# Optimization experiments

Measured on AMD Instinct MI355X. Metric: run time of the kernel, lower is better.

The kernel has to match this reference:

```python
import jax, jax.numpy as jnp
import numpy as np
import math


def setup_inputs() -> dict:
    key = jax.random.key(0)
    ks = jax.random.split(key, 4)
    B, C, H, W, D = 16, 512, 64, 64, 256
    return {
        "x": jax.random.normal(ks[0], (B, C, H, W), jnp.float32),
        "weight_global": jax.random.normal(ks[1], (C, D), jnp.float32) * 0.02,  # trunc_normal std=0.02
        "conv_g_w": jax.random.normal(ks[2], (C, C), jnp.float32) * 0.02,       # 1x1 conv, no bias
        "bn_g_gamma": jnp.ones((C,), jnp.float32),
        "bn_g_beta": jnp.zeros((C,), jnp.float32),
        "conv_c_w": jax.random.normal(ks[3], (C, C), jnp.float32) * 0.02,
        "bn_c_gamma": jnp.ones((C,), jnp.float32),
        "bn_c_beta": jnp.zeros((C,), jnp.float32),
    }


def _bn(x, gamma, beta, eps=1e-5):
    # BatchNorm2d in default training mode: batch statistics over (B, H, W)
    mean = x.mean(axis=(0, 2, 3), keepdims=True)
    var = x.var(axis=(0, 2, 3), keepdims=True)
    xn = (x - mean) * jax.lax.rsqrt(var + eps)
    return xn * gamma[None, :, None, None] + beta[None, :, None, None]


def reference(x, weight_global, conv_g_w, bn_g_gamma, bn_g_beta, conv_c_w, bn_c_gamma, bn_c_beta):
    b, c, h, w = x.shape
    inv_sqrt_c = 1.0 / math.sqrt(c)

    # Description: QR-orthogonal codebook, Q: (c, d)
    Q, _ = jnp.linalg.qr(weight_global + 1e-8)

    # global branch: 1x1 conv -> BN -> ReLU -> global avg pool
    gx = jnp.einsum('oc,bchw->bohw', conv_g_w, x)
    gx = jax.nn.relu(_bn(gx, bn_g_gamma, bn_g_beta))
    g = gx.mean(axis=(2, 3))                                  # (b, c)
    aff_g = jax.nn.softmax((g @ Q) * inv_sqrt_c, axis=1)      # (b, d)
    g = jax.nn.sigmoid(aff_g @ Q.T)                           # (b, c)

    # channel branch: 1x1 conv -> BN -> ReLU
    cx = jnp.einsum('oc,bchw->bohw', conv_c_w, x)
    cx = jax.nn.relu(_bn(cx, bn_c_gamma, bn_c_beta))
    ch = cx.reshape(b, c, h * w).transpose(0, 2, 1)           # (b, hw, c)
    aff_c = jax.nn.softmax((ch @ Q) * inv_sqrt_c, axis=2)     # (b, hw, d)
    # sum(diag_embed(aff_c) @ Q.T, dim=2) == aff_c @ Q.T (fused, avoids (b,hw,d,c) intermediate)
    ch = aff_c @ Q.T                                          # (b, hw, c)

    o = ch * g[:, None, :]
    o = o.transpose(0, 2, 1).reshape(b, c, h, w)
    return o + x
```

## Files before the change

kernel.cpp:

```cpp
#include <hip/hip_runtime.h>
#include <hip/hip_bf16.h>

#define BB 16
#define CC 512
#define HWP 4096
#define DD 256
#define NPIX 65536
#define INV_SQRT_C 0.04419417382415922f

typedef unsigned short u16;
typedef __attribute__((ext_vector_type(8))) short s16x8;
typedef __attribute__((ext_vector_type(8))) unsigned short u16x8;
typedef __attribute__((ext_vector_type(4))) unsigned short u16x4;
typedef __attribute__((ext_vector_type(4))) float f32x4;

__device__ __forceinline__ u16 f2b(float f){
  unsigned int u = __builtin_bit_cast(unsigned int, f);
  unsigned int r = (u + 0x7fffu + ((u >> 16) & 1u)) >> 16;
  return (u16)r;
}

__device__ __forceinline__ f32x4 mfma16(s16x8 a, s16x8 b, f32x4 c){
  return __builtin_amdgcn_mfma_f32_16x16x32_bf16(a, b, c, 0, 0, 0);
}

__global__ __launch_bounds__(256) void k_xbar(const float* __restrict__ x, float* __restrict__ xbar){
  int c = blockIdx.x, tid = threadIdx.x;
  float s = 0.f;
  for (int b = 0; b < BB; ++b){
    const float* px = x + ((size_t)(b*CC + c))*HWP;
    for (int p = tid; p < HWP; p += 256) s += px[p];
  }
  __shared__ float red[256];
  red[tid] = s; __syncthreads();
  for (int st = 128; st; st >>= 1){ if (tid < st) red[tid] += red[tid+st]; __syncthreads(); }
  if (tid == 0) xbar[c] = red[0] * (1.0f/ (float)NPIX);
}

__global__ __launch_bounds__(512) void k_gram(const float* __restrict__ x, float* __restrict__ Spart, int kspl){
  __shared__ __align__(16) u16 Asl[128*72];
  __shared__ __align__(16) u16 Bsl[128*72];
  int tid = threadIdx.x;
  int w = tid >> 6, lane = tid & 63, lr = lane & 15, g = lane >> 4;
  int b = blockIdx.y;
  int kz = blockIdx.z;
  int t = blockIdx.x, ti = 0, rem = 4;
  while (t >= rem){ t -= rem; ++ti; --rem; }
  int tj = ti + t;
  int r0 = ti*128, c0 = tj*128;
  int wm = w >> 2, wn = w & 3;
  f32x4 acc[4][2] = {};
  const float* xb = x + (size_t)b*CC*HWP;
  int klen = HWP / kspl;
  int kbase = kz * klen;
  for (int k0 = kbase; k0 < kbase + klen; k0 += 64){
    __syncthreads();
    for (int tt = tid; tt < 4096; tt += 512){
      int arr = tt >> 11;
      int row = (tt >> 4) & 127;
      int q = tt & 15;
      const float* src = xb + (size_t)((arr ? c0 : r0) + row)*HWP + k0 + q*4;
      f32x4 v = *(const f32x4*)src;
      u16x4 u; u[0]=f2b(v[0]); u[1]=f2b(v[1]); u[2]=f2b(v[2]); u[3]=f2b(v[3]);
      u16* dst = (arr ? Bsl : Asl) + row*72 + q*4;
      *(u16x4*)dst = u;
    }
    __syncthreads();
    #pragma unroll
    for (int kc = 0; kc < 2; ++kc){
      s16x8 av[4], bv[2];
      #pragma unroll
      for (int mt = 0; mt < 4; ++mt) av[mt] = *(const s16x8*)&Asl[(wm*64 + mt*16 + lr)*72 + kc*32 + g*8];
      #pragma unroll
      for (int nt = 0; nt < 2; ++nt) bv[nt] = *(const s16x8*)&Bsl[(wn*32 + nt*16 + lr)*72 + kc*32 + g*8];
      #pragma unroll
      for (int mt = 0; mt < 4; ++mt)
        #pragma unroll
        for (int nt = 0; nt < 2; ++nt)
          acc[mt][nt] = mfma16(av[mt], bv[nt], acc[mt][nt]);
    }
  }
  float* sp = Spart + (size_t)(b*kspl + kz)*262144;
  #pragma unroll
  for (int mt = 0; mt < 4; ++mt)
    #pragma unroll
    for (int nt = 0; nt < 2; ++nt)
      #pragma unroll
      for (int r = 0; r < 4; ++r)
        sp[(size_t)(r0 + wm*64 + mt*16 + 4*g + r)*512 + c0 + wn*32 + nt*16 + lr] = acc[mt][nt][r];
}

__global__ __launch_bounds__(256) void k_sreduce(const float* __restrict__ Spart, float* __restrict__ S, int nslots){
  int idx = blockIdx.x*256 + threadIdx.x;
  int i = idx >> 9, j = idx & 511;
  int src = ((i >> 7) <= (j >> 7)) ? idx : (j*512 + i);
  float s = 0.f;
  for (int k = 0; k < nslots; ++k) s += Spart[(size_t)k*262144 + src];
  S[idx] = s;
}

__global__ __launch_bounds__(256) void k_G(const float* __restrict__ wg, float* __restrict__ G){
  int i = blockIdx.x, j = threadIdx.x;
  float s = 0.f;
  for (int c = 0; c < CC; ++c)
    s = fmaf(wg[c*DD + i] + 1e-8f, wg[c*DD + j] + 1e-8f, s);
  G[i*DD + j] = s;
}

__global__ __launch_bounds__(256) void k_cholPanel(float* __restrict__ G, int kb){
  int tid = threadIdx.x;
  int lane = tid & 63;
  int j = lane & 31;
  int K0 = kb*32;
  float c[32];
  #pragma unroll
  for (int i = 0; i < 32; ++i)
    c[i] = (i <= j) ? G[(K0+i)*DD + K0 + j] : 0.f;
  #pragma unroll
  for (int k = 0; k < 32; ++k){
    float piv = __shfl(c[k], k);
    float sd = sqrtf(piv);
    float ukj = c[k] / sd;
    c[k] = ukj;
    float uk[32];
    #pragma unroll
    for (int i = k + 1; i < 32; ++i) uk[i] = __shfl(ukj, i);
    #pragma unroll
    for (int i = k + 1; i < 32; ++i) c[i] -= uk[i] * ukj;
  }
  if (tid < 32){
    #pragma unroll
    for (int i = 0; i < 32; ++i)
      if (i <= j) G[(K0+i)*DD + K0 + j] = c[i];
  }
  int nt = 256 - K0 - 32;
  int jg = K0 + 32 + tid;
  if (tid < nt){
    float y[32];
    #pragma unroll
    for (int i = 0; i < 32; ++i) y[i] = G[(K0+i)*DD + jg];
    #pragma unroll
    for (int i = 0; i < 32; ++i){
      float s0 = y[i];
      #pragma unroll
      for (int l = 0; l < 32; ++l)
        if (l < i) s0 -= __shfl(c[l], i) * y[l];
      y[i] = s0 / __shfl(c[i], i);
    }
    #pragma unroll
    for (int i = 0; i < 32; ++i) G[(K0+i)*DD + jg] = y[i];
  }
}

__global__ __launch_bounds__(256) void k_cholTrail(float* __restrict__ G, int kb){
  int K0 = kb*32;
  int nt = 256 - K0 - 32;
  int T = (nt + 63) >> 6;
  int t = blockIdx.x, ti = 0, rem = T;
  while (t >= rem){ t -= rem; ++ti; --rem; }
  int tj = ti + t;
  int r0 = K0 + 32 + ti*64;
  int c0 = K0 + 32 + tj*64;
  __shared__ __align__(16) float Ur[32][64];
  __shared__ __align__(16) float Uc[32][64];
  int tid = threadIdx.x;
  for (int idx = tid; idx < 2048; idx += 256){
    int k = idx >> 6, cc = idx & 63;
    int gr = r0 + cc, gc = c0 + cc;
    Ur[k][cc] = (gr < 256) ? G[(K0+k)*DD + gr] : 0.f;
    Uc[k][cc] = (gc < 256) ? G[(K0+k)*DD + gc] : 0.f;
  }
  __syncthreads();
  int tr = (tid >> 4) * 4;
  int tc = (tid & 15) * 4;
  float acc[4][4] = {};
  #pragma unroll
  for (int k = 0; k < 32; ++k){
    f32x4 a = *(const f32x4*)&Ur[k][tr];
    f32x4 b = *(const f32x4*)&Uc[k][tc];
    #pragma unroll
    for (int ii = 0; ii < 4; ++ii)
      #pragma unroll
      for (int jj = 0; jj < 4; ++jj)
        acc[ii][jj] += a[ii]*b[jj];
  }
  #pragma unroll
  for (int ii = 0; ii < 4; ++ii){
    int gi = r0 + tr + ii;
    if (gi >= 256) continue;
    #pragma unroll
    for (int jj = 0; jj < 4; ++jj){
      int gj = c0 + tc + jj;
      if (gj < 256 && gj >= gi)
        G[gi*DD + gj] -= acc[ii][jj];
    }
  }
}

__global__ __launch_bounds__(256) void k_qsolve(const float* __restrict__ G,
    const float* __restrict__ wg,
    float* __restrict__ Q, float* __restrict__ Qst,
    u16* __restrict__ Qb, u16* __restrict__ Qstb){
  __shared__ __align__(16) float Pp[8192];
  __shared__ float Qlds[256*64];
  __shared__ float Wred[3*32*64];
  int tid = threadIdx.x;
  int w = tid >> 6, lane = tid & 63;
  int c = blockIdx.x*64 + lane;
  const float* arow = wg + (size_t)c*DD;

  for (int J = 0; J < 8; ++J){
    int J0 = J*32;
    int nrows8 = (J0 + 32)*8;
    for (int idx = tid; idx < nrows8; idx += 256){
      int row = idx >> 3, q = idx & 7;
      *(f32x4*)&Pp[row*32 + q*4] = *(const f32x4*)&G[row*256 + J0 + q*4];
    }
    __syncthreads();

    float W[32];
    if (w == 0){
      #pragma unroll
      for (int r = 0; r < 32; ++r) W[r] = arow[J0 + r] + 1e-8f;
    } else {
      #pragma unroll
      for (int r = 0; r < 32; ++r) W[r] = 0.f;
    }
    for (int M = w; M < J; M += 4){
      #pragma unroll 4
      for (int k = 0; k < 32; ++k){
        int row = M*32 + k;
        float qv = Qlds[row*64 + lane];
        const float* pr = &Pp[row*32];
        #pragma unroll
        for (int r4 = 0; r4 < 8; ++r4){
          f32x4 p = *(const f32x4*)&pr[r4*4];
          W[r4*4+0] -= qv*p[0];
          W[r4*4+1] -= qv*p[1];
          W[r4*4+2] -= qv*p[2];
          W[r4*4+3] -= qv*p[3];
        }
      }
    }
    if (w > 0){
      #pragma unroll
      for (int r = 0; r < 32; ++r) Wred[((w-1)*32 + r)*64 + lane] = W[r];
    }
    __syncthreads();

    if (w == 0){
      #pragma unroll
      for (int r = 0; r < 32; ++r)
        W[r] += Wred[r*64 + lane] + Wred[(32+r)*64 + lane] + Wred[(64+r)*64 + lane];
      #pragma unroll
      for (int i = 0; i < 32; ++i){
        float t = W[i];
        for (int l = 0; l < i; ++l) t -= W[l] * Pp[(J0 + l)*32 + i];
        W[i] = t / Pp[(J0 + i)*32 + i];
      }
      #pragma unroll
      for (int i = 0; i < 32; ++i) Qlds[(J0 + i)*64 + lane] = W[i];
      #pragma unroll
      for (int r4 = 0; r4 < 8; ++r4){
        f32x4 q4; u16x4 qb4;
        #pragma unroll
        for (int jj = 0; jj < 4; ++jj){ q4[jj] = W[r4*4+jj]; qb4[jj] = f2b(W[r4*4+jj]); }
        *(f32x4*)&Q[(size_t)c*DD + J0 + r4*4] = q4;
        *(u16x4*)&Qb[(size_t)c*DD + J0 + r4*4] = qb4;
      }
      #pragma unroll
      for (int i = 0; i < 32; ++i){
        float qs = W[i] * INV_SQRT_C;
        Qst[(size_t)(J0 + i)*CC + c] = qs;
        Qstb[(size_t)(J0 + i)*CC + c] = f2b(qs);
      }
    }
    __syncthreads();
  }
}

__global__ __launch_bounds__(256) void k_fold(const float* __restrict__ Wg, const float* __restrict__ Wc,
    const float* __restrict__ gamg, const float* __restrict__ betg,
    const float* __restrict__ gamc, const float* __restrict__ betc,
    const float* __restrict__ S, const float* __restrict__ xbar,
    float* __restrict__ Wgf, float* __restrict__ bgf,
    float* __restrict__ Wcf, float* __restrict__ bcf,
    u16* __restrict__ Wgb, u16* __restrict__ Wcb){
  int o = blockIdx.x & 511, br = blockIdx.x >> 9;
  int tid = threadIdx.x;
  const float* W = br ? Wc : Wg;
  __shared__ float wrow[512];
  __shared__ float red[256];
  __shared__ float red2[256];
  __shared__ float sc_s, bi_s;
  wrow[tid] = W[o*512 + tid]; wrow[tid+256] = W[o*512 + tid + 256];
  __syncthreads();
  float mp = 0.f;
  for (int c = tid; c < 512; c += 256) mp = fmaf(wrow[c], xbar[c], mp);
  float qp = 0.f;
  for (int c1 = tid; c1 < 512; c1 += 256){
    const float* srow = S + (size_t)c1*512;
    float y = 0.f;
    for (int c2 = 0; c2 < 512; ++c2) y = fmaf(srow[c2], wrow[c2], y);
    qp = fmaf(wrow[c1], y, qp);
  }
  red[tid] = mp; red2[tid] = qp; __syncthreads();
  for (int st = 128; st; st >>= 1){
    if (tid < st){ red[tid] += red[tid+st]; red2[tid] += red2[tid+st]; }
    __syncthreads();
  }
  if (tid == 0){
    float m = red[0];
    float E = red2[0] * (1.0f/(float)NPIX);
    float var = E - m*m;
    float rstd = rsqrtf(var + 1e-5f);
    float gma = br ? gamc[o] : gamg[o];
    float bta = br ? betc[o] : betg[o];
    sc_s = gma * rstd;
    bi_s = bta - gma * rstd * m;
  }
  __syncthreads();
  float* Wf = br ? Wcf : Wgf;
  float* bf = br ? bcf : bgf;
  u16* Wb  = br ? Wcb : Wgb;
  float w0 = sc_s * wrow[tid], w1 = sc_s * wrow[tid+256];
  Wf[o*512 + tid]     = w0;
  Wf[o*512 + tid+256] = w1;
  Wb[o*512 + tid]     = f2b(w0);
  Wb[o*512 + tid+256] = f2b(w1);
  if (tid == 0) bf[o] = bi_s;
}

__global__ __launch_bounds__(512) void k_gconv(const float* __restrict__ x,
    const u16* __restrict__ Wb, const float* __restrict__ bf, float* __restrict__ gpart){
  __shared__ __align__(16) u16 Xs[64*512];
  int tid = threadIdx.x;
  int w = tid >> 6, lane = tid & 63, lr = lane & 15, g = lane >> 4;
  int slab = blockIdx.x, b = blockIdx.y;
  int p0 = slab*64;

  {
    const float* xb = x + (size_t)b*CC*HWP + p0;
    int p = tid & 63;
    int c8 = (tid >> 6) * 8;
    float v[64];
    #pragma unroll
    for (int pass = 0; pass < 8; ++pass)
      #pragma unroll
      for (int i = 0; i < 8; ++i)
        v[pass*8 + i] = xb[(size_t)(c8 + pass*64 + i)*HWP + p];
    #pragma unroll
    for (int pass = 0; pass < 8; ++pass){
      u16x8 u;
      #pragma unroll
      for (int i = 0; i < 8; ++i) u[i] = f2b(v[pass*8 + i]);
      *(u16x8*)&Xs[p*512 + ((c8 + pass*64) ^ ((p & 7) << 3))] = u;
    }
  }
  __syncthreads();

  f32x4 acc[4][4] = {};
  for (int k = 0; k < 16; ++k){
    int c0 = k*32 + g*8;
    s16x8 bv[4];
    #pragma unroll
    for (int pt = 0; pt < 4; ++pt){
      int p = pt*16 + lr;
      bv[pt] = *(const s16x8*)&Xs[p*512 + (c0 ^ ((p & 7) << 3))];
    }
    #pragma unroll
    for (int i = 0; i < 4; ++i){
      int o0 = (w*4 + i)*16;
      s16x8 a = *(const s16x8*)(Wb + (size_t)(o0 + lr)*512 + c0);
      #pragma unroll
      for (int pt = 0; pt < 4; ++pt)
        acc[i][pt] = mfma16(a, bv[pt], acc[i][pt]);
    }
  }
  #pragma unroll
  for (int i = 0; i < 4; ++i){
    int o0 = (w*4 + i)*16;
    f32x4 bias4 = *(const f32x4*)(bf + o0 + 4*g);
    float s[4] = {0.f, 0.f, 0.f, 0.f};
    #pragma unroll
    for (int pt = 0; pt < 4; ++pt)
      #pragma unroll
      for (int r = 0; r < 4; ++r)
        s[r] += fmaxf(acc[i][pt][r] + bias4[r], 0.f);
    #pragma unroll
    for (int r = 0; r < 4; ++r){
      s[r] += __shfl_xor(s[r], 1);
      s[r] += __shfl_xor(s[r], 2);
      s[r] += __shfl_xor(s[r], 4);
      s[r] += __shfl_xor(s[r], 8);
    }
    if (lr == 0){
      f32x4 sv; sv[0]=s[0]; sv[1]=s[1]; sv[2]=s[2]; sv[3]=s[3];
      *(f32x4*)(gpart + (size_t)(b*64 + slab)*512 + o0 + 4*g) = sv;
    }
  }
}

__global__ __launch_bounds__(256) void k_gvec(const float* __restrict__ gpart, const float* __restrict__ Q,
    const float* __restrict__ Qst, float* __restrict__ gvec){
  int b = blockIdx.x, tid = threadIdx.x;
  __shared__ float g0[512];
  __shared__ float aff[256];
  __shared__ float red[256];
  for (int o = tid; o < 512; o += 256){
    float s = 0.f;
    for (int sl = 0; sl < 64; ++sl) s += gpart[(size_t)(b*64 + sl)*512 + o];
    g0[o] = s * (1.0f/4096.0f);
  }
  __syncthreads();
  float l = 0.f;
  { const float* qr = Qst + (size_t)tid*512;
    for (int c = 0; c < 512; ++c) l = fmaf(qr[c], g0[c], l); }
  red[tid] = l; __syncthreads();
  for (int st = 128; st; st >>= 1){ if (tid < st) red[tid] = fmaxf(red[tid], red[tid+st]); __syncthreads(); }
  float m = red[0]; __syncthreads();
  float e = expf(l - m);
  red[tid] = e; __syncthreads();
  for (int st = 128; st; st >>= 1){ if (tid < st) red[tid] += red[tid+st]; __syncthreads(); }
  float inv = 1.0f/red[0];
  aff[tid] = e * inv;
  __syncthreads();
  for (int o = tid; o < 512; o += 256){
    const float* qr = Q + (size_t)o*DD;
    float v = 0.f;
    for (int d = 0; d < DD; ++d) v = fmaf(aff[d], qr[d], v);
    gvec[b*512 + o] = 1.0f/(1.0f + expf(-v));
  }
}

__global__ __launch_bounds__(512) void k_fused(const float* __restrict__ x,
    const u16* __restrict__ Wcb, const float* __restrict__ bcf,
    const u16* __restrict__ Qstb, const u16* __restrict__ Qb,
    const float* __restrict__ gvec, float* __restrict__ out){
  __shared__ __align__(16) u16 Xs[64*512];
  __shared__ __align__(16) u16 Ts[64*512];
  float* Lsf = (float*)Xs;
  u16*   As  = Ts;
  int tid = threadIdx.x;
  int w = tid >> 6, lane = tid & 63, lr = lane & 15, g = lane >> 4;
  int b = blockIdx.y, p0 = blockIdx.x*64;

  {
    const float* xb = x + (size_t)b*CC*HWP + p0;
    int p = tid & 63;
    int c8 = (tid >> 6) * 8;
    float v[64];
    #pragma unroll
    for (int pass = 0; pass < 8; ++pass)
      #pragma unroll
      for (int i = 0; i < 8; ++i)
        v[pass*8 + i] = xb[(size_t)(c8 + pass*64 + i)*HWP + p];
    #pragma unroll
    for (int pass = 0; pass < 8; ++pass){
      u16x8 u;
      #pragma unroll
      for (int i = 0; i < 8; ++i) u[i] = f2b(v[pass*8 + i]);
      *(u16x8*)&Xs[p*512 + ((c8 + pass*64) ^ ((p & 7) << 3))] = u;
    }
  }
  __syncthreads();

  {
    f32x4 acc[4][4] = {};
    for (int k = 0; k < 16; ++k){
      int c0 = k*32 + g*8;
      s16x8 bv[4];
      #pragma unroll
      for (int pt = 0; pt < 4; ++pt){
        int p = pt*16 + lr;
        bv[pt] = *(const s16x8*)&Xs[p*512 + (c0 ^ ((p & 7) << 3))];
      }
      #pragma unroll
      for (int i = 0; i < 4; ++i){
        int o0 = (w*4 + i)*16;
        s16x8 a = *(const s16x8*)(Wcb + (size_t)(o0 + lr)*512 + c0);
        #pragma unroll
        for (int pt = 0; pt < 4; ++pt)
          acc[i][pt] = mfma16(a, bv[pt], acc[i][pt]);
      }
    }
    #pragma unroll
    for (int i = 0; i < 4; ++i){
      int o0 = (w*4 + i)*16;
      f32x4 bias4 = *(const f32x4*)(bcf + o0 + 4*g);
      #pragma unroll
      for (int pt = 0; pt < 4; ++pt){
        int p = pt*16 + lr;
        u16x4 u;
        #pragma unroll
        for (int r = 0; r < 4; ++r) u[r] = f2b(fmaxf(acc[i][pt][r] + bias4[r], 0.f));
        *(u16x4*)&Ts[p*512 + ((o0 + 4*g) ^ ((p & 7) << 3))] = u;
      }
    }
  }
  __syncthreads();

  {
    f32x4 acc[2][4] = {};
    for (int k = 0; k < 16; ++k){
      int o0 = k*32 + g*8;
      s16x8 bv[4];
      #pragma unroll
      for (int pt = 0; pt < 4; ++pt){
        int p = pt*16 + lr;
        bv[pt] = *(const s16x8*)&Ts[p*512 + (o0 ^ ((p & 7) << 3))];
      }
      #pragma unroll
      for (int i = 0; i < 2; ++i){
        int d0 = (w*2 + i)*16;
        s16x8 a = *(const s16x8*)(Qstb + (size_t)(d0 + lr)*512 + o0);
        #pragma unroll
        for (int pt = 0; pt < 4; ++pt)
          acc[i][pt] = mfma16(a, bv[pt], acc[i][pt]);
      }
    }
    #pragma unroll
    for (int i = 0; i < 2; ++i){
      int d0 = (w*2 + i)*16;
      #pragma unroll
      for (int pt = 0; pt < 4; ++pt){
        int p = pt*16 + lr;
        *(f32x4*)&Lsf[p*256 + ((d0 + 4*g) ^ ((p & 7) << 2))] = acc[i][pt];
      }
    }
  }
  __syncthreads();

  {
    int px = tid >> 3, sub = tid & 7;
    float* Lrow = Lsf + px*256;
    int sw2 = (px & 7) << 2, sw3 = (px & 7) << 3;
    float v[32];
    #pragma unroll
    for (int jj = 0; jj < 8; ++jj){
      int d0 = sub*32 + jj*4;
      f32x4 t = *(const f32x4*)&Lrow[d0 ^ sw2];
      v[jj*4+0] = t[0]; v[jj*4+1] = t[1]; v[jj*4+2] = t[2]; v[jj*4+3] = t[3];
    }
    float m = v[0];
    #pragma unroll
    for (int jj = 1; jj < 32; ++jj) m = fmaxf(m, v[jj]);
    m = fmaxf(m, __shfl_xor(m, 1));
    m = fmaxf(m, __shfl_xor(m, 2));
    m = fmaxf(m, __shfl_xor(m, 4));
    float s = 0.f;
    #pragma unroll
    for (int jj = 0; jj < 32; ++jj){ v[jj] = __expf(v[jj] - m); s += v[jj]; }
    s += __shfl_xor(s, 1);
    s += __shfl_xor(s, 2);
    s += __shfl_xor(s, 4);
    float inv = 1.0f/s;
    #pragma unroll
    for (int jj = 0; jj < 4; ++jj){
      int d0 = sub*32 + jj*8;
      u16x8 u;
      #pragma unroll
      for (int i = 0; i < 8; ++i) u[i] = f2b(v[jj*8+i] * inv);
      *(u16x8*)&As[px*256 + (d0 ^ sw3)] = u;
    }
  }
  __syncthreads();

  {
    float xr[64];
    #pragma unroll
    for (int i = 0; i < 4; ++i)
      #pragma unroll
      for (int pt = 0; pt < 4; ++pt)
        #pragma unroll
        for (int r = 0; r < 4; ++r)
          xr[(i*4 + pt)*4 + r] =
            x[(size_t)(b*CC + (w*4 + i)*16 + 4*g + r)*HWP + p0 + pt*16 + lr];

    f32x4 acc[4][4] = {};
    for (int k = 0; k < 8; ++k){
      int d0 = k*32 + g*8;
      s16x8 bv[4];
      #pragma unroll
      for (int pt = 0; pt < 4; ++pt){
        int p = pt*16 + lr;
        bv[pt] = *(const s16x8*)&As[p*256 + (d0 ^ ((p & 7) << 3))];
      }
      #pragma unroll
      for (int i = 0; i < 4; ++i){
        int o0 = (w*4 + i)*16;
        s16x8 a = *(const s16x8*)(Qb + (size_t)(o0 + lr)*256 + d0);
        #pragma unroll
        for (int pt = 0; pt < 4; ++pt)
          acc[i][pt] = mfma16(a, bv[pt], acc[i][pt]);
      }
    }
    #pragma unroll
    for (int i = 0; i < 4; ++i){
      int o0 = (w*4 + i)*16;
      f32x4 gg = *(const f32x4*)(gvec + b*512 + o0 + 4*g);
      #pragma unroll
      for (int pt = 0; pt < 4; ++pt){
        #pragma unroll
        for (int r = 0; r < 4; ++r){
          size_t idx = (size_t)(b*CC + o0 + 4*g + r)*HWP + p0 + pt*16 + lr;
          out[idx] = fmaf(acc[i][pt][r], gg[r], xr[(i*4 + pt)*4 + r]);
        }
      }
    }
  }
}

extern "C" void kernel_launch(void* const* d_in, const int* in_sizes, int n_in,
                              void* d_out, int out_size, void* d_ws, size_t ws_size,
                              hipStream_t stream) {
  const float* x    = (const float*)d_in[0];
  const float* wg   = (const float*)d_in[1];
  const float* Wg   = (const float*)d_in[2];
  const float* gamg = (const float*)d_in[3];
  const float* betg = (const float*)d_in[4];
  const float* Wc   = (const float*)d_in[5];
  const float* gamc = (const float*)d_in[6];
  const float* betc = (const float*)d_in[7];
  float* out = (float*)d_out;

  int kspl = 1;
  {
    size_t need2 = ((size_t)1320448 + 2*16*262144 + 524288 + 393216) * 4;
    if (ws_size >= need2) kspl = 2;
  }

  float* ws = (float*)d_ws;
  float* G     = ws + 0;
  float* Q     = ws + 131072;
  float* Qst   = ws + 262144;
  float* S     = ws + 393216;
  float* xbar  = ws + 655360;
  float* Wgf   = ws + 655872;
  float* bgf   = ws + 918016;
  float* Wcf   = ws + 918528;
  float* bcf   = ws + 1180672;
  float* gvec  = ws + 1181184;
  float* Spart = ws + 1320448;
  float* gpart = Spart + (size_t)kspl*16*262144;
  u16*   ub    = (u16*)(gpart + 524288);
  u16* Qb   = ub;
  u16* Qstb = ub + 131072;
  u16* Wgb  = ub + 262144;
  u16* Wcb  = ub + 524288;

  k_xbar<<<512, 256, 0, stream>>>(x, xbar);
  k_gram<<<dim3(10,16,kspl), 512, 0, stream>>>(x, Spart, kspl);
  k_sreduce<<<1024, 256, 0, stream>>>(Spart, S, 16*kspl);
  k_G<<<256, 256, 0, stream>>>(wg, G);
  for (int kb = 0; kb < 8; ++kb){
    k_cholPanel<<<1, 256, 0, stream>>>(G, kb);
    int nt = 256 - kb*32 - 32;
    if (nt > 0){
      int T = (nt + 63) >> 6;
      k_cholTrail<<<T*(T+1)/2, 256, 0, stream>>>(G, kb);
    }
  }
  k_qsolve<<<8, 256, 0, stream>>>(G, wg, Q, Qst, Qb, Qstb);
  k_fold<<<1024, 256, 0, stream>>>(Wg, Wc, gamg, betg, gamc, betc, S, xbar, Wgf, bgf, Wcf, bcf, Wgb, Wcb);
  k_gconv<<<dim3(64,16), 512, 0, stream>>>(x, Wgb, bgf, gpart);
  k_gvec<<<16, 256, 0, stream>>>(gpart, Q, Qst, gvec);
  k_fused<<<dim3(64,16), 512, 0, stream>>>(x, Wcb, bcf, Qstb, Qb, gvec, out);
}
```

Baseline: 960.2 us.

## Use 64-wide Cholesky panels and prefetch residual x early in fused kernel

The blocked Cholesky of the codebook Gram matrix now uses 64-column panels, so the loop issues 4 panel and 3 trailing-update launches instead of 8 and 7. This cuts the number of serial tiny launches on the critical path. In exchange, each single-block panel kernel does a longer serial factorisation with 64-entry register arrays, which risks spills. Separately, the fused kernel loads the residual x values into registers at the start rather than just before the final GEMM, so those loads overlap earlier compute, at the cost of keeping 64 more live registers throughout the kernel.

```diff
diff --git a/kernel.cpp b/kernel.cpp
--- a/kernel.cpp
+++ b/kernel.cpp
@@ -107,75 +107,79 @@
   G[i*DD + j] = s;
 }
 
-__global__ __launch_bounds__(256) void k_cholPanel(float* __restrict__ G, int kb){
+__global__ __launch_bounds__(256) void k_cholPanel64(float* __restrict__ G, int kb){
   int tid = threadIdx.x;
   int lane = tid & 63;
-  int j = lane & 31;
-  int K0 = kb*32;
-  float c[32];
+  int j = lane;
+  int K0 = kb*64;
+  float c[64];
   #pragma unroll
-  for (int i = 0; i < 32; ++i)
+  for (int i = 0; i < 64; ++i)
     c[i] = (i <= j) ? G[(K0+i)*DD + K0 + j] : 0.f;
   #pragma unroll
-  for (int k = 0; k < 32; ++k){
+  for (int k = 0; k < 64; ++k){
     float piv = __shfl(c[k], k);
     float sd = sqrtf(piv);
     float ukj = c[k] / sd;
     c[k] = ukj;
-    float uk[32];
-    #pragma unroll
-    for (int i = k + 1; i < 32; ++i) uk[i] = __shfl(ukj, i);
-    #pragma unroll
-    for (int i = k + 1; i < 32; ++i) c[i] -= uk[i] * ukj;
-  }
-  if (tid < 32){
-    #pragma unroll
-    for (int i = 0; i < 32; ++i)
+    #pragma unroll
+    for (int i = k + 1; i < 64; ++i){
+      float uki = __shfl(ukj, i);
+      c[i] -= uki * ukj;
+    }
+  }
+  if (tid < 64){
+    #pragma unroll
+    for (int i = 0; i < 64; ++i)
       if (i <= j) G[(K0+i)*DD + K0 + j] = c[i];
   }
-  int nt = 256 - K0 - 32;
-  int jg = K0 + 32 + tid;
-  if (tid < nt){
-    float y[32];
-    #pragma unroll
-    for (int i = 0; i < 32; ++i) y[i] = G[(K0+i)*DD + jg];
-    #pragma unroll
-    for (int i = 0; i < 32; ++i){
+  int nt = 256 - K0 - 64;
+  if (nt > 0){
+    int jg = K0 + 64 + tid;
+    bool act = tid < nt;
+    float y[64];
+    #pragma unroll
+    for (int i = 0; i < 64; ++i) y[i] = act ? G[(K0+i)*DD + jg] : 0.f;
+    #pragma unroll
+    for (int i = 0; i < 64; ++i){
       float s0 = y[i];
       #pragma unroll
-      for (int l = 0; l < 32; ++l)
+      for (int l = 0; l < 64; ++l)
         if (l < i) s0 -= __shfl(c[l], i) * y[l];
       y[i] = s0 / __shfl(c[i], i);
     }
-    #pragma unroll
-    for (int i = 0; i < 32; ++i) G[(K0+i)*DD + jg] = y[i];
-  }
-}
-
-__global__ __launch_bounds__(256) void k_cholTrail(float* __restrict__ G, int kb){
-  int K0 = kb*32;
-  int nt = 256 - K0 - 32;
+    if (act){
+      #pragma unroll
+      for (int i = 0; i < 64; ++i) G[(K0+i)*DD + jg] = y[i];
+    }
+  }
+}
+
+__global__ __launch_bounds__(256) void k_cholTrail64(float* __restrict__ G, int kb){
+  int K0 = kb*64;
+  int nt = 256 - K0 - 64;
   int T = (nt + 63) >> 6;
   int t = blockIdx.x, ti = 0, rem = T;
   while (t >= rem){ t -= rem; ++ti; --rem; }
   int tj = ti + t;
-  int r0 = K0 + 32 + ti*64;
-  int c0 = K0 + 32 + tj*64;
-  __shared__ __align__(16) float Ur[32][64];
-  __shared__ __align__(16) float Uc[32][64];
+  int r0 = K0 + 64 + ti*64;
+  int c0 = K0 + 64 + tj*64;
+  __shared__ __align__(16) float Ur[64][64];
+  __shared__ __align__(16) float Uc[64][64];
   int tid = threadIdx.x;
-  for (int idx = tid; idx < 2048; idx += 256){
-    int k = idx >> 6, cc = idx & 63;
-    int gr = r0 + cc, gc = c0 + cc;
-    Ur[k][cc] = (gr < 256) ? G[(K0+k)*DD + gr] : 0.f;
-    Uc[k][cc] = (gc < 256) ? G[(K0+k)*DD + gc] : 0.f;
+  for (int idx = tid; idx < 8192; idx += 256){
+    int arr = idx >> 12;
+    int k = (idx >> 6) & 63, cc = idx & 63;
+    int gc = (arr ? c0 : r0) + cc;
+    float v = (gc < 256) ? G[(K0+k)*DD + gc] : 0.f;
+    if (arr) Uc[k][cc] = v; else Ur[k][cc] = v;
   }
   __syncthreads();
   int tr = (tid >> 4) * 4;
   int tc = (tid & 15) * 4;
   float acc[4][4] = {};
   #pragma unroll
-  for (int k = 0; k < 32; ++k){
+  for (int k = 0; k < 64; ++k){
     f32x4 a = *(const f32x4*)&Ur[k][tr];
     f32x4 b = *(const f32x4*)&Uc[k][tc];
     #pragma unroll
@@ -445,6 +449,7 @@
   int w = tid >> 6, lane = tid & 63, lr = lane & 15, g = lane >> 4;
   int b = blockIdx.y, p0 = blockIdx.x*64;
 
+  float xr[64];
   {
     const float* xb = x + (size_t)b*CC*HWP + p0;
     int p = tid & 63;
@@ -462,6 +467,14 @@
       for (int i = 0; i < 8; ++i) u[i] = f2b(v[pass*8 + i]);
       *(u16x8*)&Xs[p*512 + ((c8 + pass*64) ^ ((p & 7) << 3))] = u;
     }
+    #pragma unroll
+    for (int i = 0; i < 4; ++i)
+      #pragma unroll
+      for (int pt = 0; pt < 4; ++pt)
+        #pragma unroll
+        for (int r = 0; r < 4; ++r)
+          xr[(i*4 + pt)*4 + r] =
+            x[(size_t)(b*CC + (w*4 + i)*16 + 4*g + r)*HWP + p0 + pt*16 + lr];
   }
   __syncthreads();
 
@@ -567,16 +580,6 @@
   __syncthreads();
 
   {
-    float xr[64];
-    #pragma unroll
-    for (int i = 0; i < 4; ++i)
-      #pragma unroll
-      for (int pt = 0; pt < 4; ++pt)
-        #pragma unroll
-        for (int r = 0; r < 4; ++r)
-          xr[(i*4 + pt)*4 + r] =
-            x[(size_t)(b*CC + (w*4 + i)*16 + 4*g + r)*HWP + p0 + pt*16 + lr];
-
     f32x4 acc[4][4] = {};
     for (int k = 0; k < 8; ++k){
       int d0 = k*32 + g*8;
@@ -653,12 +656,12 @@
   k_gram<<<dim3(10,16,kspl), 512, 0, stream>>>(x, Spart, kspl);
   k_sreduce<<<1024, 256, 0, stream>>>(Spart, S, 16*kspl);
   k_G<<<256, 256, 0, stream>>>(wg, G);
-  for (int kb = 0; kb < 8; ++kb){
-    k_cholPanel<<<1, 256, 0, stream>>>(G, kb);
-    int nt = 256 - kb*32 - 32;
+  for (int kb = 0; kb < 4; ++kb){
+    k_cholPanel64<<<1, 256, 0, stream>>>(G, kb);
+    int nt = 256 - kb*64 - 64;
     if (nt > 0){
       int T = (nt + 63) >> 6;
-      k_cholTrail<<<T*(T+1)/2, 256, 0, stream>>>(G, kb);
+      k_cholTrail64<<<T*(T+1)/2, 256, 0, stream>>>(G, kb);
     }
   }
   k_qsolve<<<8, 256, 0, stream>>>(G, wg, Q, Qst, Qb, Qstb);
```

Result: slower. 1.518 ms (+58.1%).
